# Performance work log

Measured on AMD Instinct MI355X. Metric: run time of the kernel, lower is better.

## Reference

```python
import jax, jax.numpy as jnp
import numpy as np

EPS = 1e-5
B, C, H, W = 64, 256, 64, 64


def _masked_mean(p9, r0, r1, c0, c1):
    # p9: [B,3,3,9,H,W]; r0,r1: [B,3] int row bounds (per i); c0,c1: [B,3] int col bounds (per j)
    Hh, Ww = p9.shape[-2], p9.shape[-1]
    rows = jnp.arange(Hh, dtype=jnp.int32)
    cols = jnp.arange(Ww, dtype=jnp.int32)
    mr = (rows[None, None, :] >= r0[..., None]) & (rows[None, None, :] < r1[..., None])  # [B,3,H]
    mc = (cols[None, None, :] >= c0[..., None]) & (cols[None, None, :] < c1[..., None])  # [B,3,W]
    mask = (mr[:, :, None, :, None] & mc[:, None, :, None, :]).astype(p9.dtype)  # [B,3,3,H,W]
    cnt = mask.sum((-2, -1))  # [B,3,3]
    s = jnp.einsum('bijkhw,bijhw->bijk', p9, mask)
    return jnp.where(cnt[..., None] > 0, s / jnp.maximum(cnt, 1.0)[..., None], 0.0)  # [B,3,3,9]


def _subj_obj_bounds(bbox, Hh, Ww):
    # bbox: [B,4] = [y0,y1,x0,x1] normalized
    y0, y1, x0, x1 = bbox[:, 0], bbox[:, 1], bbox[:, 2], bbox[:, 3]
    ch = (y1 - y0) / 3.0
    cw = (x1 - x0) / 3.0
    idx = jnp.arange(3, dtype=bbox.dtype)
    r0 = jnp.floor(Hh * (y0[:, None] + idx * ch[:, None])).astype(jnp.int32)
    r1 = jnp.floor(Hh * (y0[:, None] + (idx + 1.0) * ch[:, None])).astype(jnp.int32)
    dr = r1 <= r0
    r1n = jnp.where(dr & (r1 < Hh - 1), r1 + 1, r1)
    r0n = jnp.where(dr & (r1 >= Hh - 1), r0 - 1, r0)
    c0 = jnp.floor(Ww * (x0[:, None] + idx * cw[:, None])).astype(jnp.int32)
    c1 = jnp.floor(Ww * (x0[:, None] + (idx + 1.0) * cw[:, None])).astype(jnp.int32)
    dc = c1 <= c0
    c1n = jnp.where(dc & (c1 < Ww), c1 + 1, c1)
    c0n = jnp.where(dc & (c1 >= Ww), c0 - 1, c0)
    return r0n, r1n, c0n, c1n


def _joint_bounds(bbox, bbox_s, bbox_o, Hh, Ww):
    # intersection of bbox with the 3x3 cells of union(bbox_s, bbox_o)
    uy0 = jnp.minimum(bbox_s[:, 0], bbox_o[:, 0])
    uy1 = jnp.maximum(bbox_s[:, 1], bbox_o[:, 1])
    ux0 = jnp.minimum(bbox_s[:, 2], bbox_o[:, 2])
    ux1 = jnp.maximum(bbox_s[:, 3], bbox_o[:, 3])
    ch = (uy1 - uy0) / 3.0
    cw = (ux1 - ux0) / 3.0
    idx = jnp.arange(3, dtype=bbox.dtype)
    ylo = uy0[:, None] + idx * ch[:, None]
    yhi = uy0[:, None] + (idx + 1.0) * ch[:, None]
    xlo = ux0[:, None] + idx * cw[:, None]
    xhi = ux0[:, None] + (idx + 1.0) * cw[:, None]
    r0 = jnp.floor(Hh * jnp.maximum(bbox[:, 0][:, None], ylo)).astype(jnp.int32)
    r1 = jnp.floor(Hh * jnp.minimum(bbox[:, 1][:, None], yhi)).astype(jnp.int32)
    c0 = jnp.floor(Ww * jnp.maximum(bbox[:, 2][:, None], xlo)).astype(jnp.int32)
    c1 = jnp.floor(Ww * jnp.minimum(bbox[:, 3][:, None], xhi)).astype(jnp.int32)
    return r0, r1, c0, c1


def setup_inputs() -> dict:
    key = jax.random.key(0)
    ks = jax.random.split(key, 16)
    feat = jax.random.normal(ks[0], (B, C, H, W), dtype=jnp.float32)

    def make_bbox(k):
        k1, k2, k3, k4 = jax.random.split(k, 4)
        y0 = jax.random.uniform(k1, (B,), minval=0.0, maxval=0.4)
        y1 = jnp.minimum(y0 + jax.random.uniform(k2, (B,), minval=0.3, maxval=0.55), 0.99)
        x0 = jax.random.uniform(k3, (B,), minval=0.0, maxval=0.4)
        x1 = jnp.minimum(x0 + jax.random.uniform(k4, (B,), minval=0.3, maxval=0.55), 0.99)
        return jnp.stack([y0, y1, x0, x1], axis=1).astype(jnp.float32)

    bbox_s = make_bbox(ks[1])
    bbox_o = make_bbox(ks[2])
    predicate = jax.random.uniform(ks[3], (B, 9), dtype=jnp.float32)
    conv_w = jax.random.normal(ks[4], (324, 256), dtype=jnp.float32) * 0.02
    conv_b = jax.random.normal(ks[5], (324,), dtype=jnp.float32) * 0.02
    bn2_g = jax.random.uniform(ks[6], (324,), minval=0.5, maxval=1.5)
    bn2_b = jax.random.normal(ks[7], (324,)) * 0.02
    bn2_m = jax.random.normal(ks[8], (324,)) * 0.02
    bn2_v = jax.random.uniform(ks[9], (324,), minval=0.5, maxval=1.5)
    fc1_w = jax.random.normal(ks[10], (40, 81), dtype=jnp.float32) * 0.1
    fc1_b = jnp.zeros((40,), jnp.float32)
    bn1_g = jax.random.uniform(ks[11], (40,), minval=0.5, maxval=1.5)
    bn1_b = jax.random.normal(ks[12], (40,)) * 0.02
    bn1_m = jax.random.normal(ks[13], (40,)) * 0.02
    bn1_v = jax.random.uniform(ks[14], (40,), minval=0.5, maxval=1.5)
    fc2_w = jax.random.normal(ks[15], (9, 40), dtype=jnp.float32) * 0.1
    fc2_b = jnp.zeros((9,), jnp.float32)
    return dict(feat=feat, bbox_s=bbox_s, bbox_o=bbox_o, predicate=predicate,
                conv_w=conv_w, conv_b=conv_b, bn2_g=bn2_g, bn2_b=bn2_b, bn2_m=bn2_m, bn2_v=bn2_v,
                fc1_w=fc1_w, fc1_b=fc1_b, bn1_g=bn1_g, bn1_b=bn1_b, bn1_m=bn1_m, bn1_v=bn1_v,
                fc2_w=fc2_w, fc2_b=fc2_b)


def reference(feat, bbox_s, bbox_o, predicate, conv_w, conv_b, bn2_g, bn2_b, bn2_m, bn2_v,
              fc1_w, fc1_b, bn1_g, bn1_b, bn1_m, bn1_v, fc2_w, fc2_b):
    # 1x1 conv 256 -> 324, then BatchNorm2d (inference mode)
    prs = jnp.einsum('bchw,oc->bohw', feat, conv_w) + conv_b[None, :, None, None]
    prs = (prs - bn2_m[None, :, None, None]) * (bn2_g / jnp.sqrt(bn2_v + EPS))[None, :, None, None] + bn2_b[None, :, None, None]
    Bb, _, Hh, Ww = prs.shape
    # channel layout: start = i*27 + j*9 + k  ->  reshape to [B,3,3,9,H,W]
    def bank(lo):
        return prs[:, lo:lo + 81].reshape(Bb, 3, 3, 9, Hh, Ww)
    prs_s, prs_o, prs_js, prs_jo = bank(0), bank(81), bank(162), bank(243)

    feature_s = _masked_mean(prs_s, *_subj_obj_bounds(bbox_s, Hh, Ww))
    feature_o = _masked_mean(prs_o, *_subj_obj_bounds(bbox_o, Hh, Ww))
    feature_j = (_masked_mean(prs_js, *_joint_bounds(bbox_s, bbox_s, bbox_o, Hh, Ww)) +
                 _masked_mean(prs_jo, *_joint_bounds(bbox_o, bbox_s, bbox_o, Hh, Ww)))

    f = feature_s + feature_o + feature_j            # [B,3,3,9]
    f = jnp.transpose(f, (0, 3, 1, 2)).reshape(Bb, 81)  # torch layout [B,9,3,3] flattened

    h = f @ fc1_w.T + fc1_b
    h = (h - bn1_m) * (bn1_g / jnp.sqrt(bn1_v + EPS)) + bn1_b
    logits = h @ fc2_w.T + fc2_b
    return jnp.sum(logits * predicate, axis=1)
```

## Files before the change

### kernel.cpp

```cpp
#include <hip/hip_runtime.h>
#include <hip/hip_bf16.h>
#include <cstdint>

#define BB 64
#define CC 256
#define EPSF 1e-5f
#define PLANES 4
#define ZROW 24
#define SSTR 65
#define NPLANES (BB * CC)

__device__ __forceinline__ void region_bounds(int bank, int i, int j,
                                              float sy0, float sy1, float sx0, float sx1,
                                              float oy0, float oy1, float ox0, float ox1,
                                              int& r0, int& r1, int& c0, int& c1) {
    float fi = (float)i, fj = (float)j;
    if (bank < 2) {
        float y0 = bank ? oy0 : sy0, y1 = bank ? oy1 : sy1;
        float x0 = bank ? ox0 : sx0, x1 = bank ? ox1 : sx1;
        float ch = __fdiv_rn(__fsub_rn(y1, y0), 3.0f);
        float cw = __fdiv_rn(__fsub_rn(x1, x0), 3.0f);
        int R0 = (int)floorf(__fmul_rn(64.0f, __fadd_rn(y0, __fmul_rn(fi, ch))));
        int R1 = (int)floorf(__fmul_rn(64.0f, __fadd_rn(y0, __fmul_rn(__fadd_rn(fi, 1.0f), ch))));
        bool dr = (R1 <= R0);
        r1 = (dr && (R1 < 63)) ? R1 + 1 : R1;
        r0 = (dr && (R1 >= 63)) ? R0 - 1 : R0;
        int C0 = (int)floorf(__fmul_rn(64.0f, __fadd_rn(x0, __fmul_rn(fj, cw))));
        int C1 = (int)floorf(__fmul_rn(64.0f, __fadd_rn(x0, __fmul_rn(__fadd_rn(fj, 1.0f), cw))));
        bool dc = (C1 <= C0);
        c1 = (dc && (C1 < 64)) ? C1 + 1 : C1;
        c0 = (dc && (C1 >= 64)) ? C0 - 1 : C0;
    } else {
        float by0 = (bank == 2) ? sy0 : oy0, by1 = (bank == 2) ? sy1 : oy1;
        float bx0 = (bank == 2) ? sx0 : ox0, bx1 = (bank == 2) ? sx1 : ox1;
        float uy0 = fminf(sy0, oy0), uy1 = fmaxf(sy1, oy1);
        float ux0 = fminf(sx0, ox0), ux1 = fmaxf(sx1, ox1);
        float ch = __fdiv_rn(__fsub_rn(uy1, uy0), 3.0f);
        float cw = __fdiv_rn(__fsub_rn(ux1, ux0), 3.0f);
        float ylo = __fadd_rn(uy0, __fmul_rn(fi, ch));
        float yhi = __fadd_rn(uy0, __fmul_rn(__fadd_rn(fi, 1.0f), ch));
        float xlo = __fadd_rn(ux0, __fmul_rn(fj, cw));
        float xhi = __fadd_rn(ux0, __fmul_rn(__fadd_rn(fj, 1.0f), cw));
        r0 = (int)floorf(__fmul_rn(64.0f, fmaxf(by0, ylo)));
        r1 = (int)floorf(__fmul_rn(64.0f, fminf(by1, yhi)));
        c0 = (int)floorf(__fmul_rn(64.0f, fmaxf(bx0, xlo)));
        c1 = (int)floorf(__fmul_rn(64.0f, fminf(bx1, xhi)));
    }
}

__global__ __launch_bounds__(64, 4) void k_region_sums(const float* __restrict__ feat,
                                                       const float* __restrict__ bbox_s,
                                                       const float* __restrict__ bbox_o,
                                                       float* __restrict__ M) {
    int l = threadIdx.x;
    int pid0 = blockIdx.x * PLANES;
    int b = pid0 >> 8;

    float sy0 = bbox_s[b * 4 + 0], sy1 = bbox_s[b * 4 + 1];
    float sx0 = bbox_s[b * 4 + 2], sx1 = bbox_s[b * 4 + 3];
    float oy0 = bbox_o[b * 4 + 0], oy1 = bbox_o[b * 4 + 1];
    float ox0 = bbox_o[b * 4 + 2], ox1 = bbox_o[b * 4 + 3];

    int myb = l / 9, rest = l % 9, myi = rest / 3, myj = rest % 3;

    unsigned long long needm = 0ull, snapm = 0ull;
    int my_r0c = 0, my_r1c = 0, mycl = 0, mych = 0;
    bool colact = false;
    #pragma unroll
    for (int bk = 0; bk < 4; ++bk) {
        #pragma unroll
        for (int idx = 0; idx < 3; ++idx) {
            int r0, r1, c0, c1;
            region_bounds(bk, idx, idx, sy0, sy1, sx0, sx1, oy0, oy1, ox0, ox1,
                          r0, r1, c0, c1);
            int r0c = max(r0, 0), r1c = min(r1, 64);
            if (r1c > r0c) {
                unsigned long long hi = (r1c >= 64) ? ~0ull : ((1ull << r1c) - 1ull);
                unsigned long long lo = (1ull << r0c) - 1ull;
                needm |= hi ^ lo;
                snapm |= 1ull << (r1c - 1);
                if (r0c >= 1) snapm |= 1ull << (r0c - 1);
            }
            int clc = max(c0, 0), chc = min(c1, 64);
            if (chc > clc) colact = colact || (l >= clc && l < chc);
            if (bk == myb && idx == myi) { my_r0c = r0c; my_r1c = r1c; }
            if (bk == myb && idx == myj) { mycl = max(c0, 0); mych = min(c1, 64); }
        }
    }
    {
        unsigned int a = __builtin_amdgcn_readfirstlane((unsigned int)needm);
        unsigned int bm = __builtin_amdgcn_readfirstlane((unsigned int)(needm >> 32));
        needm = (((unsigned long long)bm) << 32) | a;
        unsigned int c = __builtin_amdgcn_readfirstlane((unsigned int)snapm);
        unsigned int d = __builtin_amdgcn_readfirstlane((unsigned int)(snapm >> 32));
        snapm = (((unsigned long long)d) << 32) | c;
    }

    int cl = 0, chx = 0, idx0 = ZROW, idx1 = ZROW;
    if (l < 36) {
        cl = mycl; chx = mych;
        if (my_r1c <= my_r0c) {
            chx = cl;
        } else {
            idx1 = (int)__popcll(snapm & ((1ull << (my_r1c - 1)) - 1ull));
            idx0 = (my_r0c > 0) ? (int)__popcll(snapm & ((1ull << (my_r0c - 1)) - 1ull))
                                : ZROW;
        }
    }

    __shared__ float S[(ZROW + 1) * SSTR];
    S[ZROW * SSTR + l] = 0.0f;
    __syncthreads();

    const float* pf = feat + (size_t)pid0 * 4096 + l;
    for (int p = 0; p < PLANES; ++p) {
        float x[32];
        float run = 0.0f;
        int slot = 0;

        #pragma unroll
        for (int h = 0; h < 32; ++h) {
            float v = 0.0f;
            if (((needm >> h) & 1ull) && colact) v = pf[h * 64];
            x[h] = v;
        }
        #pragma unroll
        for (int h = 0; h < 32; ++h) {
            if ((needm >> h) & 1ull) run += x[h];
            if ((snapm >> h) & 1ull) { S[slot * SSTR + l] = run; ++slot; }
        }
        #pragma unroll
        for (int h = 0; h < 32; ++h) {
            float v = 0.0f;
            if (((needm >> (h + 32)) & 1ull) && colact) v = pf[(h + 32) * 64];
            x[h] = v;
        }
        #pragma unroll
        for (int h = 0; h < 32; ++h) {
            if ((needm >> (h + 32)) & 1ull) run += x[h];
            if ((snapm >> (h + 32)) & 1ull) { S[slot * SSTR + l] = run; ++slot; }
        }
        __syncthreads();

        if (l < 36) {
            float s = 0.0f;
            for (int w = cl; w < chx; ++w)
                s += S[idx1 * SSTR + w] - S[idx0 * SSTR + w];
            M[(size_t)l * NPLANES + pid0 + p] = s;
        }
        __syncthreads();
        pf += 4096;
    }
}

__global__ __launch_bounds__(128) void k_head_dot(const float* __restrict__ M,
                                                  const float* __restrict__ bbox_s,
                                                  const float* __restrict__ bbox_o,
                                                  const float* __restrict__ conv_w,
                                                  const float* __restrict__ conv_b,
                                                  const float* __restrict__ g2,
                                                  const float* __restrict__ b2,
                                                  const float* __restrict__ m2,
                                                  const float* __restrict__ v2,
                                                  float* __restrict__ val) {
    int blk = blockIdx.x;
    int b = blk >> 2, bank = blk & 3;
    int t = threadIdx.x;

    __shared__ float MlT9[9 * 264];
    for (int i = t; i < 9 * 256; i += 128) {
        int ij = i >> 8, c = i & 255;
        MlT9[ij * 264 + c] = M[(size_t)(bank * 9 + ij) * NPLANES + (b << 8) + c];
    }
    __syncthreads();

    if (t < 81) {
        int ij = t / 9, k = t - ij * 9;
        int ii = ij / 3, jj = ij % 3;
        int o = bank * 81 + ii * 27 + jj * 9 + k;

        float sy0 = bbox_s[b * 4 + 0], sy1 = bbox_s[b * 4 + 1];
        float sx0 = bbox_s[b * 4 + 2], sx1 = bbox_s[b * 4 + 3];
        float oy0 = bbox_o[b * 4 + 0], oy1 = bbox_o[b * 4 + 1];
        float ox0 = bbox_o[b * 4 + 2], ox1 = bbox_o[b * 4 + 3];
        int r0, r1, c0, c1;
        region_bounds(bank, ii, jj, sy0, sy1, sx0, sx1, oy0, oy1, ox0, ox1,
                      r0, r1, c0, c1);
        int nrows = max(0, min(r1, 64) - max(r0, 0));
        int ncols = max(0, min(c1, 64) - max(c0, 0));
        float cnt = (float)(nrows * ncols);

        float v = 0.0f;
        if (cnt > 0.0f) {
            const float4* wv = (const float4*)(conv_w + o * 256);
            const float4* mv = (const float4*)(&MlT9[ij * 264]);
            float4 a4 = make_float4(0.f, 0.f, 0.f, 0.f);
            #pragma unroll 8
            for (int c4 = 0; c4 < 64; ++c4) {
                float4 wq = wv[c4], mq = mv[c4];
                a4.x += wq.x * mq.x; a4.y += wq.y * mq.y;
                a4.z += wq.z * mq.z; a4.w += wq.w * mq.w;
            }
            float dot = (a4.x + a4.y) + (a4.z + a4.w);
            float mean = dot / cnt;
            float sc = g2[o] / sqrtf(v2[o] + EPSF);
            v = (mean + conv_b[o] - m2[o]) * sc + b2[o];
        }
        val[b * 324 + bank * 81 + t] = v;
    }
}

__global__ __launch_bounds__(128) void k_head_mlp(const float* __restrict__ val,
                                                  const float* __restrict__ fc1_w,
                                                  const float* __restrict__ fc1_b,
                                                  const float* __restrict__ g1,
                                                  const float* __restrict__ b1,
                                                  const float* __restrict__ m1,
                                                  const float* __restrict__ v1,
                                                  const float* __restrict__ fc2_w,
                                                  const float* __restrict__ fc2_b,
                                                  const float* __restrict__ pred,
                                                  float* __restrict__ out) {
    int b = blockIdx.x;
    int t = threadIdx.x;

    __shared__ float fv[81];
    __shared__ float hv[40];
    __shared__ float lg[9];

    if (t < 81) {
        int k = t / 9, ij = t - k * 9;
        const float* vb = val + b * 324;
        fv[t] = vb[0 * 81 + ij * 9 + k] + vb[1 * 81 + ij * 9 + k] +
                vb[2 * 81 + ij * 9 + k] + vb[3 * 81 + ij * 9 + k];
    }
    __syncthreads();

    if (t < 40) {
        float h = fc1_b[t];
        for (int u = 0; u < 81; ++u) h += fv[u] * fc1_w[t * 81 + u];
        h = (h - m1[t]) * (g1[t] / sqrtf(v1[t] + EPSF)) + b1[t];
        hv[t] = h;
    }
    __syncthreads();

    if (t < 9) {
        float lgt = fc2_b[t];
        for (int u = 0; u < 40; ++u) lgt += hv[u] * fc2_w[t * 40 + u];
        lg[t] = lgt * pred[b * 9 + t];
    }
    __syncthreads();

    if (t == 0) {
        float s = 0.0f;
        for (int i = 0; i < 9; ++i) s += lg[i];
        out[b] = s;
    }
}

extern "C" void kernel_launch(void* const* d_in, const int* in_sizes, int n_in,
                              void* d_out, int out_size, void* d_ws, size_t ws_size,
                              hipStream_t stream) {
    const float* feat   = (const float*)d_in[0];
    const float* bbox_s = (const float*)d_in[1];
    const float* bbox_o = (const float*)d_in[2];
    const float* pred   = (const float*)d_in[3];
    const float* conv_w = (const float*)d_in[4];
    const float* conv_b = (const float*)d_in[5];
    const float* g2     = (const float*)d_in[6];
    const float* b2     = (const float*)d_in[7];
    const float* m2     = (const float*)d_in[8];
    const float* v2     = (const float*)d_in[9];
    const float* fc1_w  = (const float*)d_in[10];
    const float* fc1_b  = (const float*)d_in[11];
    const float* g1     = (const float*)d_in[12];
    const float* b1     = (const float*)d_in[13];
    const float* m1     = (const float*)d_in[14];
    const float* v1     = (const float*)d_in[15];
    const float* fc2_w  = (const float*)d_in[16];
    const float* fc2_b  = (const float*)d_in[17];
    float* out = (float*)d_out;

    char* ws = (char*)d_ws;
    float* M   = (float*)ws;
    float* val = (float*)(ws + 2359296);

    k_region_sums<<<(BB * CC) / PLANES, 64, 0, stream>>>(feat, bbox_s, bbox_o, M);
    k_head_dot<<<BB * 4, 128, 0, stream>>>(M, bbox_s, bbox_o, conv_w, conv_b,
                                           g2, b2, m2, v2, val);
    k_head_mlp<<<BB, 128, 0, stream>>>(val, fc1_w, fc1_b, g1, b1, m1, v1,
                                       fc2_w, fc2_b, pred, out);
}
```

Before: 54.75 us.

## Precompute region bounds once per batch, prefetch planes, use DPP scan for column sums

Adds a small kernel that computes row/column masks, snapshot indices and counts once per batch item and stores them in a workspace table, which the region-sum and head kernels read instead of recomputing bounds. The region-sum kernel double-buffers plane loads, issuing the next plane while the current one is consumed. It replaces the serial column loop with a DPP wavefront prefix scan, so each region sum needs four shared-memory reads. The M layout is transposed so each plane's 36 results are written contiguously. The extra kernel launch and the DPP scans run at every snapshot row, and two 32-element buffers raise register pressure.

```diff
diff --git a/kernel.cpp b/kernel.cpp
--- a/kernel.cpp
+++ b/kernel.cpp
@@ -9,6 +9,7 @@
 #define ZROW 24
 #define SSTR 65
 #define NPLANES (BB * CC)
+#define BDSTR 128
 
 __device__ __forceinline__ void region_bounds(int bank, int i, int j,
                                               float sy0, float sy1, float sx0, float sx1,
@@ -48,114 +49,185 @@
     }
 }
 
+__global__ __launch_bounds__(64) void k_bounds(const float* __restrict__ bbox_s,
+                                               const float* __restrict__ bbox_o,
+                                               uint32_t* __restrict__ bd) {
+    int b = blockIdx.x, t = threadIdx.x;
+    __shared__ unsigned int msk[6];
+    if (t < 6) msk[t] = 0u;
+    __syncthreads();
+
+    float sy0 = bbox_s[b * 4 + 0], sy1 = bbox_s[b * 4 + 1];
+    float sx0 = bbox_s[b * 4 + 2], sx1 = bbox_s[b * 4 + 3];
+    float oy0 = bbox_o[b * 4 + 0], oy1 = bbox_o[b * 4 + 1];
+    float ox0 = bbox_o[b * 4 + 2], ox1 = bbox_o[b * 4 + 3];
+
+    if (t < 12) {
+        int bank = t / 3, idx = t % 3;
+        int r0, r1, c0, c1;
+        region_bounds(bank, idx, idx, sy0, sy1, sx0, sx1, oy0, oy1, ox0, ox1,
+                      r0, r1, c0, c1);
+        int r0c = min(max(r0, 0), 64), r1c = min(max(r1, 0), 64);
+        if (r1c > r0c) {
+            unsigned long long rows =
+                ((r1c >= 64) ? ~0ull : ((1ull << r1c) - 1ull)) ^ ((1ull << r0c) - 1ull);
+            atomicOr(&msk[0], (unsigned)rows);
+            atomicOr(&msk[1], (unsigned)(rows >> 32));
+            unsigned long long sn = 1ull << (r1c - 1);
+            if (r0c >= 1) sn |= 1ull << (r0c - 1);
+            atomicOr(&msk[2], (unsigned)sn);
+            atomicOr(&msk[3], (unsigned)(sn >> 32));
+        }
+        int c0c = min(max(c0, 0), 64), c1c = min(max(c1, 0), 64);
+        if (c1c > c0c) {
+            unsigned long long cols =
+                ((c1c >= 64) ? ~0ull : ((1ull << c1c) - 1ull)) ^ ((1ull << c0c) - 1ull);
+            atomicOr(&msk[4], (unsigned)cols);
+            atomicOr(&msk[5], (unsigned)(cols >> 32));
+        }
+    }
+    __syncthreads();
+
+    unsigned long long snapm = (((unsigned long long)msk[3]) << 32) | msk[2];
+    if (t < 36) {
+        int bank = t / 9, ij = t % 9, ii = ij / 3, jj = ij % 3;
+        int r0, r1, c0, c1;
+        region_bounds(bank, ii, jj, sy0, sy1, sx0, sx1, oy0, oy1, ox0, ox1,
+                      r0, r1, c0, c1);
+        int r0c = min(max(r0, 0), 64), r1c = min(max(r1, 0), 64);
+        int clc = min(max(c0, 0), 64), chc = min(max(c1, 0), 64);
+        int nrows = max(0, r1c - r0c), ncols = max(0, chc - clc);
+        float cnt = (float)(nrows * ncols);
+        int i0 = ZROW, i1 = ZROW;
+        if (r1c > r0c) {
+            i1 = (int)__popcll(snapm & ((1ull << (r1c - 1)) - 1ull));
+            i0 = (r0c > 0) ? (int)__popcll(snapm & ((1ull << (r0c - 1)) - 1ull)) : ZROW;
+        }
+        bd[b * BDSTR + 4 + t] = (unsigned)clc | ((unsigned)chc << 8) |
+                                ((unsigned)i0 << 16) | ((unsigned)i1 << 24);
+        bd[b * BDSTR + 40 + t] = __float_as_uint(cnt);
+    }
+    if (t < 4) bd[b * BDSTR + t] = msk[t];
+    if (t == 4 || t == 5) bd[b * BDSTR + 72 + t] = msk[t];
+}
+
+__device__ __forceinline__ float dpp_scan_incl(float v) {
+    float t;
+    t = __int_as_float(__builtin_amdgcn_update_dpp(0, __float_as_int(v), 0x111, 0xf, 0xf, true));  v += t;
+    t = __int_as_float(__builtin_amdgcn_update_dpp(0, __float_as_int(v), 0x112, 0xf, 0xf, true));  v += t;
+    t = __int_as_float(__builtin_amdgcn_update_dpp(0, __float_as_int(v), 0x114, 0xf, 0xf, true));  v += t;
+    t = __int_as_float(__builtin_amdgcn_update_dpp(0, __float_as_int(v), 0x118, 0xf, 0xf, true));  v += t;
+    t = __int_as_float(__builtin_amdgcn_update_dpp(0, __float_as_int(v), 0x142, 0xa, 0xf, false)); v += t;
+    t = __int_as_float(__builtin_amdgcn_update_dpp(0, __float_as_int(v), 0x143, 0xc, 0xf, false)); v += t;
+    return v;
+}
+
 __global__ __launch_bounds__(64, 4) void k_region_sums(const float* __restrict__ feat,
-                                                       const float* __restrict__ bbox_s,
-                                                       const float* __restrict__ bbox_o,
+                                                       const uint32_t* __restrict__ bd,
                                                        float* __restrict__ M) {
     int l = threadIdx.x;
     int pid0 = blockIdx.x * PLANES;
     int b = pid0 >> 8;
 
-    float sy0 = bbox_s[b * 4 + 0], sy1 = bbox_s[b * 4 + 1];
-    float sx0 = bbox_s[b * 4 + 2], sx1 = bbox_s[b * 4 + 3];
-    float oy0 = bbox_o[b * 4 + 0], oy1 = bbox_o[b * 4 + 1];
-    float ox0 = bbox_o[b * 4 + 2], ox1 = bbox_o[b * 4 + 3];
-
-    int myb = l / 9, rest = l % 9, myi = rest / 3, myj = rest % 3;
-
-    unsigned long long needm = 0ull, snapm = 0ull;
-    int my_r0c = 0, my_r1c = 0, mycl = 0, mych = 0;
-    bool colact = false;
+    const uint32_t* bdp = bd + b * BDSTR;
+    unsigned long long needm, snapm, colm;
+    {
+        unsigned int n0 = __builtin_amdgcn_readfirstlane(bdp[0]);
+        unsigned int n1 = __builtin_amdgcn_readfirstlane(bdp[1]);
+        unsigned int s0 = __builtin_amdgcn_readfirstlane(bdp[2]);
+        unsigned int s1 = __builtin_amdgcn_readfirstlane(bdp[3]);
+        unsigned int c0 = __builtin_amdgcn_readfirstlane(bdp[76]);
+        unsigned int c1 = __builtin_amdgcn_readfirstlane(bdp[77]);
+        needm = (((unsigned long long)n1) << 32) | n0;
+        snapm = (((unsigned long long)s1) << 32) | s0;
+        colm  = (((unsigned long long)c1) << 32) | c0;
+    }
+    bool colact = ((colm >> l) & 1ull) != 0ull;
+
+    uint32_t pk = bdp[4 + l];
+    int cl   = pk & 255;
+    int chx  = (pk >> 8) & 255;
+    int idx0 = (pk >> 16) & 255;
+    int idx1 = (pk >> 24) & 255;
+
+    __shared__ float S[(ZROW + 1) * SSTR];
+    if (l < ZROW + 1) S[l * SSTR] = 0.0f;
+    S[ZROW * SSTR + 1 + l] = 0.0f;
+    __syncthreads();
+
+    float xA[32], xB[32];
+
+#define ISSUE(P)                                                            \
+    do {                                                                    \
+        const float* pp = feat + (size_t)(pid0 + (P)) * 4096 + l;           \
+        _Pragma("unroll")                                                   \
+        for (int h = 0; h < 32; ++h) {                                      \
+            if ((needm >> h) & 1ull) {                                      \
+                float v = 0.0f;                                             \
+                if (colact) v = pp[h * 64];                                 \
+                xA[h] = v;                                                  \
+            }                                                               \
+        }                                                                   \
+        _Pragma("unroll")                                                   \
+        for (int h = 0; h < 32; ++h) {                                      \
+            if ((needm >> (h + 32)) & 1ull) {                               \
+                float v = 0.0f;                                             \
+                if (colact) v = pp[(h + 32) * 64];                          \
+                xB[h] = v;                                                  \
+            }                                                               \
+        }                                                                   \
+    } while (0)
+
+#define CONSUME()                                                           \
+    do {                                                                    \
+        float run = 0.0f;                                                   \
+        int slot = 0;                                                       \
+        _Pragma("unroll")                                                   \
+        for (int h = 0; h < 32; ++h) {                                      \
+            if ((needm >> h) & 1ull) run += xA[h];                          \
+            if ((snapm >> h) & 1ull) {                                      \
+                S[slot * SSTR + 1 + l] = dpp_scan_incl(run);                \
+                ++slot;                                                     \
+            }                                                               \
+        }                                                                   \
+        _Pragma("unroll")                                                   \
+        for (int h = 0; h < 32; ++h) {                                      \
+            if ((needm >> (h + 32)) & 1ull) run += xB[h];                   \
+            if ((snapm >> (h + 32)) & 1ull) {                               \
+                S[slot * SSTR + 1 + l] = dpp_scan_incl(run);                \
+                ++slot;                                                     \
+            }                                                               \
+        }                                                                   \
+    } while (0)
+
+#define EVAL(P)                                                             \
+    do {                                                                    \
+        if (l < 36) {                                                       \
+            float s = S[idx1 * SSTR + chx] - S[idx1 * SSTR + cl] -          \
+                      S[idx0 * SSTR + chx] + S[idx0 * SSTR + cl];           \
+            M[(size_t)(pid0 + (P)) * 36 + l] = s;                           \
+        }                                                                   \
+    } while (0)
+
+    ISSUE(0);
     #pragma unroll
-    for (int bk = 0; bk < 4; ++bk) {
-        #pragma unroll
-        for (int idx = 0; idx < 3; ++idx) {
-            int r0, r1, c0, c1;
-            region_bounds(bk, idx, idx, sy0, sy1, sx0, sx1, oy0, oy1, ox0, ox1,
-                          r0, r1, c0, c1);
-            int r0c = max(r0, 0), r1c = min(r1, 64);
-            if (r1c > r0c) {
-                unsigned long long hi = (r1c >= 64) ? ~0ull : ((1ull << r1c) - 1ull);
-                unsigned long long lo = (1ull << r0c) - 1ull;
-                needm |= hi ^ lo;
-                snapm |= 1ull << (r1c - 1);
-                if (r0c >= 1) snapm |= 1ull << (r0c - 1);
-            }
-            int clc = max(c0, 0), chc = min(c1, 64);
-            if (chc > clc) colact = colact || (l >= clc && l < chc);
-            if (bk == myb && idx == myi) { my_r0c = r0c; my_r1c = r1c; }
-            if (bk == myb && idx == myj) { mycl = max(c0, 0); mych = min(c1, 64); }
-        }
-    }
-    {
-        unsigned int a = __builtin_amdgcn_readfirstlane((unsigned int)needm);
-        unsigned int bm = __builtin_amdgcn_readfirstlane((unsigned int)(needm >> 32));
-        needm = (((unsigned long long)bm) << 32) | a;
-        unsigned int c = __builtin_amdgcn_readfirstlane((unsigned int)snapm);
-        unsigned int d = __builtin_amdgcn_readfirstlane((unsigned int)(snapm >> 32));
-        snapm = (((unsigned long long)d) << 32) | c;
-    }
-
-    int cl = 0, chx = 0, idx0 = ZROW, idx1 = ZROW;
-    if (l < 36) {
-        cl = mycl; chx = mych;
-        if (my_r1c <= my_r0c) {
-            chx = cl;
-        } else {
-            idx1 = (int)__popcll(snapm & ((1ull << (my_r1c - 1)) - 1ull));
-            idx0 = (my_r0c > 0) ? (int)__popcll(snapm & ((1ull << (my_r0c - 1)) - 1ull))
-                                : ZROW;
-        }
-    }
-
-    __shared__ float S[(ZROW + 1) * SSTR];
-    S[ZROW * SSTR + l] = 0.0f;
-    __syncthreads();
-
-    const float* pf = feat + (size_t)pid0 * 4096 + l;
     for (int p = 0; p < PLANES; ++p) {
-        float x[32];
-        float run = 0.0f;
-        int slot = 0;
-
-        #pragma unroll
-        for (int h = 0; h < 32; ++h) {
-            float v = 0.0f;
-            if (((needm >> h) & 1ull) && colact) v = pf[h * 64];
-            x[h] = v;
-        }
-        #pragma unroll
-        for (int h = 0; h < 32; ++h) {
-            if ((needm >> h) & 1ull) run += x[h];
-            if ((snapm >> h) & 1ull) { S[slot * SSTR + l] = run; ++slot; }
-        }
-        #pragma unroll
-        for (int h = 0; h < 32; ++h) {
-            float v = 0.0f;
-            if (((needm >> (h + 32)) & 1ull) && colact) v = pf[(h + 32) * 64];
-            x[h] = v;
-        }
-        #pragma unroll
-        for (int h = 0; h < 32; ++h) {
-            if ((needm >> (h + 32)) & 1ull) run += x[h];
-            if ((snapm >> (h + 32)) & 1ull) { S[slot * SSTR + l] = run; ++slot; }
-        }
+        CONSUME();
+        if (p == 0) ISSUE(1);
+        if (p == 1) ISSUE(2);
+        if (p == 2) ISSUE(3);
         __syncthreads();
-
-        if (l < 36) {
-            float s = 0.0f;
-            for (int w = cl; w < chx; ++w)
-                s += S[idx1 * SSTR + w] - S[idx0 * SSTR + w];
-            M[(size_t)l * NPLANES + pid0 + p] = s;
-        }
+        EVAL(p);
         __syncthreads();
-        pf += 4096;
-    }
+    }
+
+#undef ISSUE
+#undef CONSUME
+#undef EVAL
 }
 
 __global__ __launch_bounds__(128) void k_head_dot(const float* __restrict__ M,
-                                                  const float* __restrict__ bbox_s,
-                                                  const float* __restrict__ bbox_o,
+                                                  const uint32_t* __restrict__ bd,
                                                   const float* __restrict__ conv_w,
                                                   const float* __restrict__ conv_b,
                                                   const float* __restrict__ g2,
@@ -170,7 +242,7 @@
     __shared__ float MlT9[9 * 264];
     for (int i = t; i < 9 * 256; i += 128) {
         int ij = i >> 8, c = i & 255;
-        MlT9[ij * 264 + c] = M[(size_t)(bank * 9 + ij) * NPLANES + (b << 8) + c];
+        MlT9[ij * 264 + c] = M[(size_t)(b * 256 + c) * 36 + bank * 9 + ij];
     }
     __syncthreads();
 
@@ -178,17 +250,7 @@
         int ij = t / 9, k = t - ij * 9;
         int ii = ij / 3, jj = ij % 3;
         int o = bank * 81 + ii * 27 + jj * 9 + k;
-
-        float sy0 = bbox_s[b * 4 + 0], sy1 = bbox_s[b * 4 + 1];
-        float sx0 = bbox_s[b * 4 + 2], sx1 = bbox_s[b * 4 + 3];
-        float oy0 = bbox_o[b * 4 + 0], oy1 = bbox_o[b * 4 + 1];
-        float ox0 = bbox_o[b * 4 + 2], ox1 = bbox_o[b * 4 + 3];
-        int r0, r1, c0, c1;
-        region_bounds(bank, ii, jj, sy0, sy1, sx0, sx1, oy0, oy1, ox0, ox1,
-                      r0, r1, c0, c1);
-        int nrows = max(0, min(r1, 64) - max(r0, 0));
-        int ncols = max(0, min(c1, 64) - max(c0, 0));
-        float cnt = (float)(nrows * ncols);
+        float cnt = __uint_as_float(bd[b * BDSTR + 40 + bank * 9 + ij]);
 
         float v = 0.0f;
         if (cnt > 0.0f) {
@@ -282,12 +344,13 @@
     float* out = (float*)d_out;
 
     char* ws = (char*)d_ws;
-    float* M   = (float*)ws;
-    float* val = (float*)(ws + 2359296);
-
-    k_region_sums<<<(BB * CC) / PLANES, 64, 0, stream>>>(feat, bbox_s, bbox_o, M);
-    k_head_dot<<<BB * 4, 128, 0, stream>>>(M, bbox_s, bbox_o, conv_w, conv_b,
-                                           g2, b2, m2, v2, val);
+    float*    M   = (float*)ws;
+    uint32_t* bdb = (uint32_t*)(ws + 2359296);
+    float*    val = (float*)(ws + 2359296 + 32768);
+
+    k_bounds<<<BB, 64, 0, stream>>>(bbox_s, bbox_o, bdb);
+    k_region_sums<<<(BB * CC) / PLANES, 64, 0, stream>>>(feat, bdb, M);
+    k_head_dot<<<BB * 4, 128, 0, stream>>>(M, bdb, conv_w, conv_b, g2, b2, m2, v2, val);
     k_head_mlp<<<BB, 128, 0, stream>>>(val, fc1_w, fc1_b, g1, b1, m1, v1,
                                        fc2_w, fc2_b, pred, out);
 }
```

Result: slower. 63.72 us (+16.4%).

## Fuse head dot and MLP kernels; redirect inactive-column loads to a needed column

Applied to the files above, without the earlier changes.

Merges the two head kernels into one per-batch kernel with 384 threads that stages all 36 region sums in shared memory, computes the 324 conv/BN values, then runs the MLP, removing one launch and the global round trip for the intermediate values. In the region-sum kernel, lanes whose column is not needed now load from a column that is needed instead of branching on colact, so the loads carry no divergent predicate and all fall on cache lines already being fetched. Values read by inactive lanes are still summed into shared memory, but only columns inside each region's range are read back. The head now runs only 64 blocks, which lowers its parallelism.

```diff
diff --git a/kernel.cpp b/kernel.cpp
--- a/kernel.cpp
+++ b/kernel.cpp
@@ -66,6 +66,7 @@
     unsigned long long needm = 0ull, snapm = 0ull;
     int my_r0c = 0, my_r1c = 0, mycl = 0, mych = 0;
     bool colact = false;
+    int cmin = 64;
     #pragma unroll
     for (int bk = 0; bk < 4; ++bk) {
         #pragma unroll
@@ -82,7 +83,10 @@
                 if (r0c >= 1) snapm |= 1ull << (r0c - 1);
             }
             int clc = max(c0, 0), chc = min(c1, 64);
-            if (chc > clc) colact = colact || (l >= clc && l < chc);
+            if (chc > clc) {
+                colact = colact || (l >= clc && l < chc);
+                cmin = min(cmin, clc);
+            }
             if (bk == myb && idx == myi) { my_r0c = r0c; my_r1c = r1c; }
             if (bk == myb && idx == myj) { mycl = max(c0, 0); mych = min(c1, 64); }
         }
@@ -95,6 +99,8 @@
         unsigned int d = __builtin_amdgcn_readfirstlane((unsigned int)(snapm >> 32));
         snapm = (((unsigned long long)d) << 32) | c;
     }
+    if (cmin >= 64) cmin = 0;
+    int col_tgt = colact ? l : cmin;
 
     int cl = 0, chx = 0, idx0 = ZROW, idx1 = ZROW;
     if (l < 36) {
@@ -112,7 +118,7 @@
     S[ZROW * SSTR + l] = 0.0f;
     __syncthreads();
 
-    const float* pf = feat + (size_t)pid0 * 4096 + l;
+    const float* pf = feat + (size_t)pid0 * 4096 + col_tgt;
     for (int p = 0; p < PLANES; ++p) {
         float x[32];
         float run = 0.0f;
@@ -120,9 +126,7 @@
 
         #pragma unroll
         for (int h = 0; h < 32; ++h) {
-            float v = 0.0f;
-            if (((needm >> h) & 1ull) && colact) v = pf[h * 64];
-            x[h] = v;
+            if ((needm >> h) & 1ull) x[h] = pf[h * 64];
         }
         #pragma unroll
         for (int h = 0; h < 32; ++h) {
@@ -131,9 +135,7 @@
         }
         #pragma unroll
         for (int h = 0; h < 32; ++h) {
-            float v = 0.0f;
-            if (((needm >> (h + 32)) & 1ull) && colact) v = pf[(h + 32) * 64];
-            x[h] = v;
+            if ((needm >> (h + 32)) & 1ull) x[h] = pf[(h + 32) * 64];
         }
         #pragma unroll
         for (int h = 0; h < 32; ++h) {
@@ -153,29 +155,43 @@
     }
 }
 
-__global__ __launch_bounds__(128) void k_head_dot(const float* __restrict__ M,
-                                                  const float* __restrict__ bbox_s,
-                                                  const float* __restrict__ bbox_o,
-                                                  const float* __restrict__ conv_w,
-                                                  const float* __restrict__ conv_b,
-                                                  const float* __restrict__ g2,
-                                                  const float* __restrict__ b2,
-                                                  const float* __restrict__ m2,
-                                                  const float* __restrict__ v2,
-                                                  float* __restrict__ val) {
-    int blk = blockIdx.x;
-    int b = blk >> 2, bank = blk & 3;
+__global__ __launch_bounds__(384) void k_head(const float* __restrict__ M,
+                                              const float* __restrict__ bbox_s,
+                                              const float* __restrict__ bbox_o,
+                                              const float* __restrict__ conv_w,
+                                              const float* __restrict__ conv_b,
+                                              const float* __restrict__ g2,
+                                              const float* __restrict__ b2,
+                                              const float* __restrict__ m2,
+                                              const float* __restrict__ v2,
+                                              const float* __restrict__ fc1_w,
+                                              const float* __restrict__ fc1_b,
+                                              const float* __restrict__ g1,
+                                              const float* __restrict__ b1,
+                                              const float* __restrict__ m1,
+                                              const float* __restrict__ v1,
+                                              const float* __restrict__ fc2_w,
+                                              const float* __restrict__ fc2_b,
+                                              const float* __restrict__ pred,
+                                              float* __restrict__ out) {
+    int b = blockIdx.x;
     int t = threadIdx.x;
 
-    __shared__ float MlT9[9 * 264];
-    for (int i = t; i < 9 * 256; i += 128) {
-        int ij = i >> 8, c = i & 255;
-        MlT9[ij * 264 + c] = M[(size_t)(bank * 9 + ij) * NPLANES + (b << 8) + c];
-    }
-    __syncthreads();
-
-    if (t < 81) {
-        int ij = t / 9, k = t - ij * 9;
+    __shared__ float MlT[36 * 264];
+    __shared__ float val[324];
+    __shared__ float fv[81];
+    __shared__ float hv[40];
+    __shared__ float lg[9];
+
+    for (int i = t; i < 36 * 256; i += 384) {
+        int r = i >> 8, c = i & 255;
+        MlT[r * 264 + c] = M[(size_t)r * NPLANES + (b << 8) + c];
+    }
+    __syncthreads();
+
+    if (t < 324) {
+        int region = t / 9, k = t - region * 9;
+        int bank = region / 9, ij = region - bank * 9;
         int ii = ij / 3, jj = ij % 3;
         int o = bank * 81 + ii * 27 + jj * 9 + k;
 
@@ -193,7 +209,7 @@
         float v = 0.0f;
         if (cnt > 0.0f) {
             const float4* wv = (const float4*)(conv_w + o * 256);
-            const float4* mv = (const float4*)(&MlT9[ij * 264]);
+            const float4* mv = (const float4*)(&MlT[region * 264]);
             float4 a4 = make_float4(0.f, 0.f, 0.f, 0.f);
             #pragma unroll 8
             for (int c4 = 0; c4 < 64; ++c4) {
@@ -206,33 +222,14 @@
             float sc = g2[o] / sqrtf(v2[o] + EPSF);
             v = (mean + conv_b[o] - m2[o]) * sc + b2[o];
         }
-        val[b * 324 + bank * 81 + t] = v;
-    }
-}
-
-__global__ __launch_bounds__(128) void k_head_mlp(const float* __restrict__ val,
-                                                  const float* __restrict__ fc1_w,
-                                                  const float* __restrict__ fc1_b,
-                                                  const float* __restrict__ g1,
-                                                  const float* __restrict__ b1,
-                                                  const float* __restrict__ m1,
-                                                  const float* __restrict__ v1,
-                                                  const float* __restrict__ fc2_w,
-                                                  const float* __restrict__ fc2_b,
-                                                  const float* __restrict__ pred,
-                                                  float* __restrict__ out) {
-    int b = blockIdx.x;
-    int t = threadIdx.x;
-
-    __shared__ float fv[81];
-    __shared__ float hv[40];
-    __shared__ float lg[9];
+        val[t] = v;
+    }
+    __syncthreads();
 
     if (t < 81) {
         int k = t / 9, ij = t - k * 9;
-        const float* vb = val + b * 324;
-        fv[t] = vb[0 * 81 + ij * 9 + k] + vb[1 * 81 + ij * 9 + k] +
-                vb[2 * 81 + ij * 9 + k] + vb[3 * 81 + ij * 9 + k];
+        fv[t] = val[0 * 81 + ij * 9 + k] + val[1 * 81 + ij * 9 + k] +
+                val[2 * 81 + ij * 9 + k] + val[3 * 81 + ij * 9 + k];
     }
     __syncthreads();
 
@@ -281,13 +278,10 @@
     const float* fc2_b  = (const float*)d_in[17];
     float* out = (float*)d_out;
 
-    char* ws = (char*)d_ws;
-    float* M   = (float*)ws;
-    float* val = (float*)(ws + 2359296);
+    float* M = (float*)d_ws;
 
     k_region_sums<<<(BB * CC) / PLANES, 64, 0, stream>>>(feat, bbox_s, bbox_o, M);
-    k_head_dot<<<BB * 4, 128, 0, stream>>>(M, bbox_s, bbox_o, conv_w, conv_b,
-                                           g2, b2, m2, v2, val);
-    k_head_mlp<<<BB, 128, 0, stream>>>(val, fc1_w, fc1_b, g1, b1, m1, v1,
-                                       fc2_w, fc2_b, pred, out);
-}
+    k_head<<<BB, 384, 0, stream>>>(M, bbox_s, bbox_o, conv_w, conv_b, g2, b2, m2, v2,
+                                   fc1_w, fc1_b, g1, b1, m1, v1, fc2_w, fc2_b,
+                                   pred, out);
+}
```

After: 56.24 us. 1.03x slower.

## Software-pipeline plane loads with double buffers and drop block barriers in region sums

Applied to the files above, without the earlier changes.

Doubles the planes handled per block and rewrites the per-plane loop as a manually unrolled double-buffered pipeline. Loads for the next half-plane are issued while the current half is being prefix-summed. The block is a single wavefront of 64 threads, so __syncthreads is replaced with lgkmcnt waits. Inactive columns now load a valid in-range column instead of being predicated off, which removes the branch but adds some redundant memory traffic. The explicit waits instead of barriers depend on wave-level LDS ordering, and the larger unrolled register footprint may lower occupancy.

```diff
diff --git a/kernel.cpp b/kernel.cpp
--- a/kernel.cpp
+++ b/kernel.cpp
@@ -5,7 +5,7 @@
 #define BB 64
 #define CC 256
 #define EPSF 1e-5f
-#define PLANES 4
+#define PLANES 8
 #define ZROW 24
 #define SSTR 65
 #define NPLANES (BB * CC)
@@ -66,6 +66,7 @@
     unsigned long long needm = 0ull, snapm = 0ull;
     int my_r0c = 0, my_r1c = 0, mycl = 0, mych = 0;
     bool colact = false;
+    int cmin = 64;
     #pragma unroll
     for (int bk = 0; bk < 4; ++bk) {
         #pragma unroll
@@ -82,7 +83,10 @@
                 if (r0c >= 1) snapm |= 1ull << (r0c - 1);
             }
             int clc = max(c0, 0), chc = min(c1, 64);
-            if (chc > clc) colact = colact || (l >= clc && l < chc);
+            if (chc > clc) {
+                colact = colact || (l >= clc && l < chc);
+                cmin = min(cmin, clc);
+            }
             if (bk == myb && idx == myi) { my_r0c = r0c; my_r1c = r1c; }
             if (bk == myb && idx == myj) { mycl = max(c0, 0); mych = min(c1, 64); }
         }
@@ -95,6 +99,8 @@
         unsigned int d = __builtin_amdgcn_readfirstlane((unsigned int)(snapm >> 32));
         snapm = (((unsigned long long)d) << 32) | c;
     }
+    if (cmin >= 64) cmin = 0;
+    int col_tgt = colact ? l : cmin;
 
     int cl = 0, chx = 0, idx0 = ZROW, idx1 = ZROW;
     if (l < 36) {
@@ -110,47 +116,67 @@
 
     __shared__ float S[(ZROW + 1) * SSTR];
     S[ZROW * SSTR + l] = 0.0f;
-    __syncthreads();
-
-    const float* pf = feat + (size_t)pid0 * 4096 + l;
-    for (int p = 0; p < PLANES; ++p) {
-        float x[32];
-        float run = 0.0f;
-        int slot = 0;
-
-        #pragma unroll
-        for (int h = 0; h < 32; ++h) {
-            float v = 0.0f;
-            if (((needm >> h) & 1ull) && colact) v = pf[h * 64];
-            x[h] = v;
-        }
-        #pragma unroll
-        for (int h = 0; h < 32; ++h) {
-            if ((needm >> h) & 1ull) run += x[h];
-            if ((snapm >> h) & 1ull) { S[slot * SSTR + l] = run; ++slot; }
-        }
-        #pragma unroll
-        for (int h = 0; h < 32; ++h) {
-            float v = 0.0f;
-            if (((needm >> (h + 32)) & 1ull) && colact) v = pf[(h + 32) * 64];
-            x[h] = v;
-        }
-        #pragma unroll
-        for (int h = 0; h < 32; ++h) {
-            if ((needm >> (h + 32)) & 1ull) run += x[h];
-            if ((snapm >> (h + 32)) & 1ull) { S[slot * SSTR + l] = run; ++slot; }
-        }
-        __syncthreads();
-
-        if (l < 36) {
-            float s = 0.0f;
-            for (int w = cl; w < chx; ++w)
-                s += S[idx1 * SSTR + w] - S[idx0 * SSTR + w];
-            M[(size_t)l * NPLANES + pid0 + p] = s;
-        }
-        __syncthreads();
-        pf += 4096;
-    }
+    asm volatile("s_waitcnt lgkmcnt(0)" ::: "memory");
+
+    const float* pfbase = feat + (size_t)pid0 * 4096 + col_tgt;
+    float xA[32], xB[32];
+    float run = 0.0f;
+    int slot = 0;
+
+#define ISSUE_H(X, Q)                                                       \
+    do {                                                                    \
+        const float* pp = pfbase + (size_t)((Q) >> 1) * 4096;               \
+        const int h0 = ((Q) & 1) * 32;                                      \
+        _Pragma("unroll")                                                   \
+        for (int h = 0; h < 32; ++h) {                                      \
+            if ((needm >> (h0 + h)) & 1ull) X[h] = pp[(h0 + h) * 64];       \
+        }                                                                   \
+    } while (0)
+
+#define CONSUME_H(X, Q)                                                     \
+    do {                                                                    \
+        const int h0 = ((Q) & 1) * 32;                                      \
+        if (h0 == 0) { run = 0.0f; slot = 0; }                              \
+        _Pragma("unroll")                                                   \
+        for (int h = 0; h < 32; ++h) {                                      \
+            if ((needm >> (h0 + h)) & 1ull) run += X[h];                    \
+            if ((snapm >> (h0 + h)) & 1ull) { S[slot * SSTR + l] = run; ++slot; } \
+        }                                                                   \
+    } while (0)
+
+#define EVALP(P)                                                            \
+    do {                                                                    \
+        asm volatile("s_waitcnt lgkmcnt(0)" ::: "memory");                  \
+        if (l < 36) {                                                       \
+            float s = 0.0f;                                                 \
+            for (int w = cl; w < chx; ++w)                                  \
+                s += S[idx1 * SSTR + w] - S[idx0 * SSTR + w];               \
+            M[(size_t)l * NPLANES + pid0 + (P)] = s;                        \
+        }                                                                   \
+        asm volatile("" ::: "memory");                                      \
+    } while (0)
+
+    ISSUE_H(xA, 0); ISSUE_H(xB, 1);
+    CONSUME_H(xA, 0);  ISSUE_H(xA, 2);
+    CONSUME_H(xB, 1);  ISSUE_H(xB, 3);   EVALP(0);
+    CONSUME_H(xA, 2);  ISSUE_H(xA, 4);
+    CONSUME_H(xB, 3);  ISSUE_H(xB, 5);   EVALP(1);
+    CONSUME_H(xA, 4);  ISSUE_H(xA, 6);
+    CONSUME_H(xB, 5);  ISSUE_H(xB, 7);   EVALP(2);
+    CONSUME_H(xA, 6);  ISSUE_H(xA, 8);
+    CONSUME_H(xB, 7);  ISSUE_H(xB, 9);   EVALP(3);
+    CONSUME_H(xA, 8);  ISSUE_H(xA, 10);
+    CONSUME_H(xB, 9);  ISSUE_H(xB, 11);  EVALP(4);
+    CONSUME_H(xA, 10); ISSUE_H(xA, 12);
+    CONSUME_H(xB, 11); ISSUE_H(xB, 13);  EVALP(5);
+    CONSUME_H(xA, 12); ISSUE_H(xA, 14);
+    CONSUME_H(xB, 13); ISSUE_H(xB, 15);  EVALP(6);
+    CONSUME_H(xA, 14);
+    CONSUME_H(xB, 15);                   EVALP(7);
+
+#undef ISSUE_H
+#undef CONSUME_H
+#undef EVALP
 }
 
 __global__ __launch_bounds__(128) void k_head_dot(const float* __restrict__ M,
```

After: 61.90 us. +13.1%, slower.
